# Kernel optimization log

Measured on AMD Instinct MI355X. Metric: run time of the kernel, lower is better.

The kernel has to match this reference:

```python
import jax, jax.numpy as jnp
import numpy as np

B, T, D, R = 4, 2048, 1024, 64

def setup_inputs() -> dict:
    key = jax.random.key(0)
    ks = jax.random.split(key, 13)
    x = jax.random.normal(ks[0], (B, T, D), jnp.float32)
    # Linear weights stored torch-style [out, in]; applied as x @ W.T
    WQ = jax.random.normal(ks[1], (D, D), jnp.float32) * 0.02
    WK = jax.random.normal(ks[2], (D, D), jnp.float32) * 0.02
    WO = jax.random.normal(ks[3], (D, D), jnp.float32) * 0.02
    Winv = jnp.eye(D, dtype=jnp.float32) + 0.01 * jax.random.normal(ks[4], (D, D), jnp.float32)
    U_b = jax.random.normal(ks[5], (D, R), jnp.float32) * 0.02
    V_b = jax.random.normal(ks[6], (D, R), jnp.float32) * 0.02
    W_b = jax.random.normal(ks[7], (D, R), jnp.float32) * 0.02
    bias_b = jnp.zeros((D,), jnp.float32)
    U_t = jax.random.normal(ks[8], (D, R), jnp.float32) * 0.02
    V_t = jax.random.normal(ks[9], (D, R), jnp.float32) * 0.02
    W_t = jax.random.normal(ks[10], (D, R), jnp.float32) * 0.02
    X_t = jax.random.normal(ks[11], (D, R), jnp.float32) * 0.02
    bias_t = jnp.zeros((D,), jnp.float32)
    alpha_bi = jnp.float32(0.5)
    alpha_tri = jnp.float32(0.5)
    return {"x": x, "WQ": WQ, "WK": WK, "WO": WO, "Winv": Winv,
            "U_b": U_b, "V_b": V_b, "W_b": W_b, "bias_b": bias_b,
            "U_t": U_t, "V_t": V_t, "W_t": W_t, "X_t": X_t, "bias_t": bias_t,
            "alpha_bi": alpha_bi, "alpha_tri": alpha_tri}


def reference(x, WQ, WK, WO, Winv, U_b, V_b, W_b, bias_b,
              U_t, V_t, W_t, X_t, bias_t, alpha_bi, alpha_tri):
    # Faithful forward. The original materializes [B,T,T,D] pairwise tensors,
    # masks causally, sums over j and divides by n_valid. Because the (i,j)
    # score factorizes as f(i)*g(j) in rank space, sum_{j<=i} == f(i)*cumsum(g)_i,
    # so we use causal cumulative sums -- identical math, O(B*T*D*R) memory.
    Tlen = x.shape[1]
    Q = x @ WQ.T                       # [B,T,D]
    K = x @ WK.T
    invQ = Q @ Winv.T
    invK = K @ Winv.T
    counts = jnp.arange(1, Tlen + 1, dtype=x.dtype)[None, :, None]  # [1,T,1]
    z = jnp.cumsum(x, axis=1) / counts  # causal global mean, [B,T,D]
    # bilinear forward: sum_{j<=i} ((Q_i V_b) * (K_j W_b)) U_b^T + bias_b
    fwd_r = (Q @ V_b) * jnp.cumsum(K @ W_b, axis=1)          # [B,T,R]
    # bilinear inverse: sum_{j<=i} ((invK_j V_b) * (invQ_i W_b)) U_b^T + bias_b
    inv_r = jnp.cumsum(invK @ V_b, axis=1) * (invQ @ W_b)    # [B,T,R]
    # trilinear: sum_{j<=i} ((Q_i V_t)*(K_j W_t)*(Z_i X_t)) U_t^T + bias_t
    tri_r = (Q @ V_t) * jnp.cumsum(K @ W_t, axis=1) * (z @ X_t)  # [B,T,R]
    sum_fwd = fwd_r @ U_b.T + counts * bias_b                # [B,T,D]
    sum_inv = inv_r @ U_b.T + counts * bias_b
    sum_tri = tri_r @ U_t.T + counts * bias_t
    out = (sum_fwd + alpha_bi * sum_inv + alpha_tri * sum_tri) / counts
    return out @ WO.T
```

## Files before the change

### kernel.cpp

```cpp
#include <hip/hip_runtime.h>

#define T_LEN 2048
#define BT_DIM 8192

typedef __attribute__((ext_vector_type(8))) short s16x8;
typedef __attribute__((ext_vector_type(4))) float f32x4;

typedef __attribute__((address_space(1))) void gvoid_t;
typedef __attribute__((address_space(3))) void svoid_t;

__device__ __forceinline__ unsigned short f2bf(float f) {
  unsigned int u = __builtin_bit_cast(unsigned int, f);
  u += 0x7fffu + ((u >> 16) & 1u);
  return (unsigned short)(u >> 16);
}
__device__ __forceinline__ float bf2f(unsigned short u) {
  unsigned int v = (unsigned int)u << 16;
  return __builtin_bit_cast(float, v);
}
__device__ __forceinline__ void gload16(const void* g, void* l) {
  __builtin_amdgcn_global_load_lds((gvoid_t*)g, (svoid_t*)l, 16, 0, 0);
}

template<int EPI>
__device__ __forceinline__ void gemm_body(
    const unsigned short* __restrict__ A, const unsigned short* __restrict__ B,
    void* __restrict__ Cv, int lda, int ldb, int ldc, int K, int m0, int n0,
    const float* __restrict__ obias, float* __restrict__ sums, int ygrp,
    int rlo, int rhi)
{
  __shared__ unsigned short As[2 * 128 * 64];
  __shared__ unsigned short Bs[2 * 128 * 64];
  const int tid  = threadIdx.x;
  const int wave = tid >> 6;
  const int lane = tid & 63;
  const int wr = wave >> 1, wc = wave & 1;
  const int trow = tid >> 3;
  const int scol = (((tid & 7) ^ ((tid >> 3) & 7)) << 3);

  const unsigned short* Ap = A + (size_t)(m0 + trow) * lda + scol;
  const unsigned short* Bp = B + (size_t)(n0 + trow) * ldb + scol;

  f32x4 acc[4][4] = {};

  auto stage = [&](int buf, int kt) {
    char* ab = (char*)As + buf * 16384 + wave * 1024;
    char* bb = (char*)Bs + buf * 16384 + wave * 1024;
#pragma unroll
    for (int it = 0; it < 4; ++it) {
      gload16(Ap + (size_t)it * 32 * lda + kt, ab + it * 4096);
      gload16(Bp + (size_t)it * 32 * ldb + kt, bb + it * 4096);
    }
  };

  stage(0, 0);
  __syncthreads();
  int cur = 0;
  const int xr = (lane & 7) << 3;
  for (int kt = 64; kt <= K; kt += 64) {
    if (kt < K) stage(cur ^ 1, kt);
#pragma unroll
    for (int ks = 0; ks < 2; ++ks) {
      const int kk = ((ks << 5) + ((lane >> 4) << 3)) ^ xr;
      const int ra = (wr << 6) + (lane & 15);
      const int rb = (wc << 6) + (lane & 15);
      s16x8 af[4], bfr[4];
#pragma unroll
      for (int i = 0; i < 4; ++i)
        af[i] = *(const s16x8*)&As[cur * 8192 + (ra + (i << 4)) * 64 + kk];
#pragma unroll
      for (int i = 0; i < 4; ++i)
        bfr[i] = *(const s16x8*)&Bs[cur * 8192 + (rb + (i << 4)) * 64 + kk];
#pragma unroll
      for (int i = 0; i < 4; ++i)
#pragma unroll
        for (int j = 0; j < 4; ++j)
          acc[i][j] = __builtin_amdgcn_mfma_f32_16x16x32_bf16(af[i], bfr[j], acc[i][j], 0, 0, 0);
    }
    __syncthreads();
    cur ^= 1;
  }

  if (EPI == 2) {
    unsigned short* C = (unsigned short*)Cv;
#pragma unroll
    for (int i = 0; i < 4; ++i) {
      const int lr0 = (wr << 6) + (i << 4) + ((lane >> 4) << 2);
#pragma unroll
      for (int j = 0; j < 4; ++j) {
        const int c = n0 + (wc << 6) + (j << 4) + (lane & 15);
#pragma unroll
        for (int rr = 0; rr < 4; ++rr) {
          const int lr = lr0 + rr;
          if (lr >= rlo && lr < rhi)
            C[(size_t)(m0 + lr) * ldc + c] = f2bf(acc[i][j][rr]);
        }
      }
    }
  } else if (EPI == 3) {
    float* C = (float*)Cv;
    float ob[4];
#pragma unroll
    for (int j = 0; j < 4; ++j)
      ob[j] = obias[n0 + (wc << 6) + (j << 4) + (lane & 15)];
#pragma unroll
    for (int i = 0; i < 4; ++i) {
      const int r0 = m0 + (wr << 6) + (i << 4) + ((lane >> 4) << 2);
#pragma unroll
      for (int j = 0; j < 4; ++j) {
        const int c = n0 + (wc << 6) + (j << 4) + (lane & 15);
#pragma unroll
        for (int rr = 0; rr < 4; ++rr)
          C[(size_t)(r0 + rr) * ldc + c] = acc[i][j][rr] + ob[j];
      }
    }
  } else {
    unsigned short* C = (unsigned short*)Cv;
#pragma unroll
    for (int i = 0; i < 4; ++i) {
      const int r0 = m0 + (wr << 6) + (i << 4) + ((lane >> 4) << 2);
#pragma unroll
      for (int j = 0; j < 4; ++j) {
        const int c = (wc << 6) + (j << 4) + (lane & 15);
#pragma unroll
        for (int rr = 0; rr < 4; ++rr)
          C[(size_t)(r0 + rr) * ldc + c] = f2bf(acc[i][j][rr]);
      }
    }
    int soff = -1;
    if (ygrp == 1) soff = wc << 6;
    else if (ygrp == 2 && wc == 0) soff = 128;
    else if (ygrp == 3 && wc == 0) soff = 192;
    if (soff >= 0) {
#pragma unroll
      for (int i = 0; i < 4; ++i) {
        const int R0 = m0 + (wr << 6) + (i << 4);
        const int b_ = R0 >> 11, ch = (R0 & 2047) >> 4;
#pragma unroll
        for (int j = 0; j < 4; ++j) {
          float v = acc[i][j][0] + acc[i][j][1] + acc[i][j][2] + acc[i][j][3];
          v += __shfl_xor(v, 16);
          v += __shfl_xor(v, 32);
          if (lane < 16)
            sums[(((b_ << 7) + ch) << 8) + soff + (j << 4) + lane] = v;
        }
      }
    }
  }
}

__global__ __launch_bounds__(256) void smallA_k(
    const unsigned short* BQ, const unsigned short* BK, const unsigned short* BI,
    const unsigned short* WOb, const unsigned short* WQt, const unsigned short* WKt,
    const unsigned short* Winvt, const unsigned short* UcatT,
    unsigned short* Gcat, unsigned short* Hb, unsigned short* Gfin)
{
  const int bx = blockIdx.x;
  const unsigned short *A, *B; unsigned short* C; int ldc, m0, n0;
  switch (blockIdx.y) {
    case 0:  A = BQ;  B = WQt;   C = Gcat;              ldc = 1024; m0 = 0; n0 = bx * 128; break;
    case 1:  A = BK;  B = WKt;   C = Gcat + 128 * 1024; ldc = 1024; m0 = 0; n0 = bx * 128; break;
    case 2:  A = BI;  B = Winvt; C = Hb;                ldc = 1024; m0 = 0; n0 = bx * 128; break;
    default: A = WOb; B = UcatT; C = Gfin;              ldc = 128;  m0 = bx * 128; n0 = 0; break;
  }
  gemm_body<2>(A, B, C, 1024, 1024, ldc, 1024, m0, n0, nullptr, nullptr, 0, 0, 128);
}

__global__ __launch_bounds__(256) void smallB_k(
    const unsigned short* Hb, const unsigned short* WKt, const unsigned short* WQt,
    unsigned short* Gcat)
{
  const int bx = blockIdx.x;
  const unsigned short* B = (blockIdx.y == 0) ? WKt : WQt;
  const int rlo = (blockIdx.y == 0) ? 0 : 64;
  gemm_body<2>(Hb, B, Gcat + 256 * 1024, 1024, 1024, 1024, 1024, 0, bx * 128,
               nullptr, nullptr, 0, rlo, rlo + 64);
}

__global__ __launch_bounds__(256) void mainP_k(
    const unsigned short* __restrict__ xb, const unsigned short* __restrict__ Gcat,
    unsigned short* __restrict__ Pcat, float* __restrict__ sums)
{
  const int y = blockIdx.y, kz = blockIdx.z;
  gemm_body<4>(xb + kz * 512, Gcat + (size_t)y * 128 * 1024 + kz * 512,
               Pcat + (size_t)kz * BT_DIM * 512 + y * 128,
               1024, 1024, 512, 512, blockIdx.x * 128, 0,
               nullptr, sums + kz * 131072, y, 0, 128);
}

__global__ __launch_bounds__(256) void final_k(
    const unsigned short* __restrict__ rcat, const unsigned short* __restrict__ Gfin,
    const float* __restrict__ obias, float* __restrict__ out)
{
  gemm_body<3>(rcat, Gfin, out, 128, 128, 1024, 128,
               blockIdx.x * 128, blockIdx.y * 128, obias, nullptr, 0, 0, 128);
}

__global__ __launch_bounds__(256) void prep_k(
    const float* __restrict__ x, const float* __restrict__ WQ,
    const float* __restrict__ WK, const float* __restrict__ WO,
    const float* __restrict__ Winv, const float* __restrict__ U_b,
    const float* __restrict__ V_b, const float* __restrict__ W_b,
    const float* __restrict__ bias_b, const float* __restrict__ U_t,
    const float* __restrict__ V_t, const float* __restrict__ W_t,
    const float* __restrict__ X_t, const float* __restrict__ bias_t,
    const float* __restrict__ abi_p, const float* __restrict__ atri_p,
    unsigned short* xb, unsigned short* WQt, unsigned short* WKt,
    unsigned short* Winvt, unsigned short* WOb, unsigned short* BQ,
    unsigned short* BK, unsigned short* BI, unsigned short* UcatT,
    unsigned short* Gcat, float* obias)
{
  __shared__ float smem[64 * 65];
  const int bx = blockIdx.x, tid = threadIdx.x;
  if (bx < 8192) {
    int i = bx * 256 + tid;
    float4 v = ((const float4*)x)[i];
    ushort4 o; o.x = f2bf(v.x); o.y = f2bf(v.y); o.z = f2bf(v.z); o.w = f2bf(v.w);
    ((ushort4*)xb)[i] = o;
  } else if (bx < 8960) {
    int local = bx - 8192;
    const float* s; unsigned short* d;
    switch (local >> 8) { case 0: s = WQ; d = WQt; break;
                          case 1: s = WK; d = WKt; break;
                          default: s = Winv; d = Winvt; break; }
    int t = local & 255;
    int tY = t >> 4, tX = t & 15;
    int c = tid & 63, g = tid >> 6;
#pragma unroll
    for (int rr = 0; rr < 16; ++rr) {
      int r = g * 16 + rr;
      smem[r * 65 + c] = s[(size_t)(tY * 64 + r) * 1024 + tX * 64 + c];
    }
    __syncthreads();
#pragma unroll
    for (int rr = 0; rr < 16; ++rr) {
      int r = g * 16 + rr;
      d[(size_t)(tX * 64 + r) * 1024 + tY * 64 + c] = f2bf(smem[c * 65 + r]);
    }
  } else if (bx < 10496) {
    int local = bx - 8960;
    const float *s0, *s1; unsigned short* d;
    switch (local >> 9) { case 0: s0 = V_b; s1 = V_t; d = BQ; break;
                          case 1: s0 = W_b; s1 = W_t; d = BK; break;
                          default: s0 = V_b; s1 = W_b; d = BI; break; }
    int idx = (local & 511) * 256 + tid;
    int n = idx >> 10, k = idx & 1023;
    const float* s = (n < 64) ? s0 : s1;
    d[idx] = f2bf(s[k * 64 + (n & 63)]);
  } else if (bx < 11008) {
    int idx = (bx - 10496) * 256 + tid;
    int k = idx >> 10, dd = idx & 1023;
    UcatT[idx] = f2bf(k < 64 ? U_b[dd * 64 + k] : U_t[dd * 64 + k - 64]);
  } else if (bx < 11520) {
    int idx = (bx - 11008) * 256 + tid;
    int r = idx >> 10, dd = idx & 1023;
    Gcat[(size_t)384 * 1024 + idx] = f2bf(X_t[dd * 64 + (r & 63)]);
  } else if (bx < 12544) {
    int i = (bx - 11520) * 256 + tid;
    float4 v = ((const float4*)WO)[i];
    ushort4 o; o.x = f2bf(v.x); o.y = f2bf(v.y); o.z = f2bf(v.z); o.w = f2bf(v.w);
    ((ushort4*)WOb)[i] = o;
  } else {
    int n = bx - 12544;
    const float abi = abi_p[0], atri = atri_p[0];
    float s = 0.f;
    for (int d0 = tid; d0 < 1024; d0 += 256)
      s += ((1.f + abi) * bias_b[d0] + atri * bias_t[d0]) * WO[(size_t)n * 1024 + d0];
    smem[tid] = s;
    __syncthreads();
#pragma unroll
    for (int w = 128; w > 0; w >>= 1) {
      if (tid < w) smem[tid] += smem[tid + w];
      __syncthreads();
    }
    if (tid == 0) obias[n] = smem[0];
  }
}

__global__ __launch_bounds__(256) void scanB_k(
    const unsigned short* __restrict__ P, const float* __restrict__ sums,
    const float* __restrict__ abi_p, const float* __restrict__ atri_p,
    unsigned short* __restrict__ rcat)
{
  const int w = blockIdx.x * 4 + (threadIdx.x >> 6);
  const int lane = threadIdx.x & 63;
  const int b = w >> 7, ch = w & 127;
  float c2 = 0.f, c6 = 0.f, c3 = 0.f, cZ = 0.f;
  for (int i = 0; i < ch; ++i) {
    const float* s0 = sums + ((((size_t)b << 7) + i) << 8) + lane;
    const float* s1 = s0 + 131072;
    c2 += s0[0]   + s1[0];
    c6 += s0[64]  + s1[64];
    c3 += s0[128] + s1[128];
    cZ += s0[192] + s1[192];
  }
  const float abi = abi_p[0], atri = atri_p[0];
  const size_t row0 = (size_t)b * T_LEN + ch * 16;
  const unsigned short* P1 = P + (size_t)BT_DIM * 512;
#pragma unroll 2
  for (int t = 0; t < 16; ++t) {
    const size_t ro = (row0 + t) * 512 + lane;
    const float p1 = bf2f(P[ro])       + bf2f(P1[ro]);
    const float p5 = bf2f(P[ro + 64])  + bf2f(P1[ro + 64]);
    c2            += bf2f(P[ro + 128]) + bf2f(P1[ro + 128]);
    c6            += bf2f(P[ro + 192]) + bf2f(P1[ro + 192]);
    c3            += bf2f(P[ro + 256]) + bf2f(P1[ro + 256]);
    const float p4 = bf2f(P[ro + 320]) + bf2f(P1[ro + 320]);
    cZ            += bf2f(P[ro + 384]) + bf2f(P1[ro + 384]);
    const float invc = 1.0f / (float)(ch * 16 + t + 1);
    const float rb = (p1 * c2 + abi * (c3 * p4)) * invc;
    const float rt = atri * p5 * c6 * cZ * invc * invc;
    const size_t rro = (row0 + t) * 128;
    rcat[rro + lane]      = f2bf(rb);
    rcat[rro + 64 + lane] = f2bf(rt);
  }
}

extern "C" void kernel_launch(void* const* d_in, const int* in_sizes, int n_in,
                              void* d_out, int out_size, void* d_ws, size_t ws_size,
                              hipStream_t stream)
{
  const float* x      = (const float*)d_in[0];
  const float* WQ     = (const float*)d_in[1];
  const float* WK     = (const float*)d_in[2];
  const float* WO     = (const float*)d_in[3];
  const float* Winv   = (const float*)d_in[4];
  const float* U_b    = (const float*)d_in[5];
  const float* V_b    = (const float*)d_in[6];
  const float* W_b    = (const float*)d_in[7];
  const float* bias_b = (const float*)d_in[8];
  const float* U_t    = (const float*)d_in[9];
  const float* V_t    = (const float*)d_in[10];
  const float* W_t    = (const float*)d_in[11];
  const float* X_t    = (const float*)d_in[12];
  const float* bias_t = (const float*)d_in[13];
  const float* a_bi   = (const float*)d_in[14];
  const float* a_tri  = (const float*)d_in[15];

  char* ws = (char*)d_ws;
  size_t off = 0;
  unsigned short* xb    = (unsigned short*)(ws + off); off += (size_t)BT_DIM * 1024 * 2;
  unsigned short* Pcat  = (unsigned short*)(ws + off); off += (size_t)2 * BT_DIM * 512 * 2;
  unsigned short* rcat  = (unsigned short*)(ws + off); off += (size_t)BT_DIM * 128 * 2;
  unsigned short* WQt   = (unsigned short*)(ws + off); off += 2097152;
  unsigned short* WKt   = (unsigned short*)(ws + off); off += 2097152;
  unsigned short* Winvt = (unsigned short*)(ws + off); off += 2097152;
  unsigned short* WOb   = (unsigned short*)(ws + off); off += 2097152;
  unsigned short* BQ    = (unsigned short*)(ws + off); off += 262144;
  unsigned short* BK    = (unsigned short*)(ws + off); off += 262144;
  unsigned short* BI    = (unsigned short*)(ws + off); off += 262144;
  unsigned short* Hb    = (unsigned short*)(ws + off); off += 262144;
  unsigned short* UcatT = (unsigned short*)(ws + off); off += 262144;
  unsigned short* Gcat  = (unsigned short*)(ws + off); off += (size_t)512 * 1024 * 2;
  unsigned short* Gfin  = (unsigned short*)(ws + off); off += 262144;
  float*          obias = (float*)(ws + off);          off += 4096;
  float*          sums  = (float*)(ws + off);          off += 1048576;

  prep_k<<<dim3(13568), 256, 0, stream>>>(x, WQ, WK, WO, Winv, U_b, V_b, W_b, bias_b,
                                          U_t, V_t, W_t, X_t, bias_t, a_bi, a_tri,
                                          xb, WQt, WKt, Winvt, WOb, BQ, BK, BI,
                                          UcatT, Gcat, obias);
  smallA_k<<<dim3(8, 4), 256, 0, stream>>>(BQ, BK, BI, WOb, WQt, WKt, Winvt, UcatT,
                                           Gcat, Hb, Gfin);
  smallB_k<<<dim3(8, 2), 256, 0, stream>>>(Hb, WKt, WQt, Gcat);
  mainP_k<<<dim3(64, 4, 2), 256, 0, stream>>>(xb, Gcat, Pcat, sums);
  scanB_k<<<dim3(128), 256, 0, stream>>>(Pcat, sums, a_bi, a_tri, rcat);
  final_k<<<dim3(64, 8), 256, 0, stream>>>(rcat, Gfin, obias, (float*)d_out);
}
```

Before: 219.1 us.

## Precompute chunk carries with a separate warp-shuffle scan kernel

Adds a scanC_k kernel that computes exclusive prefix sums of the per-chunk partial sums across the 128 chunks using wave shuffles, and writes them to a new carry buffer. scanB_k then reads its starting carry directly instead of each wave serially summing up to 127 previous chunk sums, which removes the quadratic serial loop. The inner row loop unroll is also raised from 2 to 4. The cost is one extra kernel launch and an extra small buffer round trip.

```diff
diff --git a/kernel.cpp b/kernel.cpp
--- a/kernel.cpp
+++ b/kernel.cpp
@@ -277,27 +277,42 @@
   }
 }
 
+__global__ __launch_bounds__(256) void scanC_k(const float* __restrict__ sums,
+                                               float* __restrict__ carry)
+{
+  const int W = blockIdx.x * 4 + (threadIdx.x >> 6);
+  const int lane = threadIdx.x & 63;
+  const int b = W >> 8, col = W & 255;
+  const int ch0 = lane << 1;
+  const size_t i0 = ((((size_t)b << 7) + ch0) << 8) + col;
+  const size_t i1 = i0 + 256;
+  const float v0 = sums[i0] + sums[i0 + 131072];
+  const float v1 = sums[i1] + sums[i1 + 131072];
+  float a = v0 + v1;
+#pragma unroll
+  for (int off = 1; off < 64; off <<= 1) {
+    const float u = __shfl_up(a, off);
+    if (lane >= off) a += u;
+  }
+  const float excl = a - (v0 + v1);
+  carry[i0] = excl;
+  carry[i1] = excl + v0;
+}
+
 __global__ __launch_bounds__(256) void scanB_k(
-    const unsigned short* __restrict__ P, const float* __restrict__ sums,
+    const unsigned short* __restrict__ P, const float* __restrict__ carry,
     const float* __restrict__ abi_p, const float* __restrict__ atri_p,
     unsigned short* __restrict__ rcat)
 {
   const int w = blockIdx.x * 4 + (threadIdx.x >> 6);
   const int lane = threadIdx.x & 63;
   const int b = w >> 7, ch = w & 127;
-  float c2 = 0.f, c6 = 0.f, c3 = 0.f, cZ = 0.f;
-  for (int i = 0; i < ch; ++i) {
-    const float* s0 = sums + ((((size_t)b << 7) + i) << 8) + lane;
-    const float* s1 = s0 + 131072;
-    c2 += s0[0]   + s1[0];
-    c6 += s0[64]  + s1[64];
-    c3 += s0[128] + s1[128];
-    cZ += s0[192] + s1[192];
-  }
+  const float* cp = carry + ((((size_t)b << 7) + ch) << 8) + lane;
+  float c2 = cp[0], c6 = cp[64], c3 = cp[128], cZ = cp[192];
   const float abi = abi_p[0], atri = atri_p[0];
   const size_t row0 = (size_t)b * T_LEN + ch * 16;
   const unsigned short* P1 = P + (size_t)BT_DIM * 512;
-#pragma unroll 2
+#pragma unroll 4
   for (int t = 0; t < 16; ++t) {
     const size_t ro = (row0 + t) * 512 + lane;
     const float p1 = bf2f(P[ro])       + bf2f(P1[ro]);
@@ -355,6 +370,7 @@
   unsigned short* Gfin  = (unsigned short*)(ws + off); off += 262144;
   float*          obias = (float*)(ws + off);          off += 4096;
   float*          sums  = (float*)(ws + off);          off += 1048576;
+  float*          carry = (float*)(ws + off);          off += 524288;
 
   prep_k<<<dim3(13568), 256, 0, stream>>>(x, WQ, WK, WO, Winv, U_b, V_b, W_b, bias_b,
                                           U_t, V_t, W_t, X_t, bias_t, a_bi, a_tri,
@@ -364,6 +380,7 @@
                                            Gcat, Hb, Gfin);
   smallB_k<<<dim3(8, 2), 256, 0, stream>>>(Hb, WKt, WQt, Gcat);
   mainP_k<<<dim3(64, 4, 2), 256, 0, stream>>>(xb, Gcat, Pcat, sums);
-  scanB_k<<<dim3(128), 256, 0, stream>>>(Pcat, sums, a_bi, a_tri, rcat);
+  scanC_k<<<dim3(256), 256, 0, stream>>>(sums, carry);
+  scanB_k<<<dim3(128), 256, 0, stream>>>(Pcat, carry, a_bi, a_tri, rcat);
   final_k<<<dim3(64, 8), 256, 0, stream>>>(rcat, Gfin, obias, (float*)d_out);
 }
```

New measurement: 194.6 us. 1.13x faster.
